# Optimization experiments

Measured on AMD Instinct MI355X. Metric: run time of the kernel, lower is better.

The kernel has to match this reference:

```python
import jax, jax.numpy as jnp
import numpy as np

N, D, M = 4096, 2048, 1000
NL = 2048
MAX_ITER = 5


def setup_inputs() -> dict:
    key = jax.random.key(0)
    k1, k2, k3 = jax.random.split(key, 3)
    fc7 = jax.random.normal(k1, (N, D), dtype=jnp.float32)
    # prior probs: softmax over random logits (row-stochastic, like CNN softmax output)
    probs = jax.nn.softmax(jax.random.normal(k2, (N, M), dtype=jnp.float32), axis=-1)
    labs = jax.random.randint(k3, (NL,), 0, M)
    L = jnp.arange(NL)
    U = jnp.arange(NL, N)
    return {"fc7": fc7, "probs": probs, "labs": labs, "L": L, "U": U}


def _get_W_correlation(fc7):
    # Pearson correlation between rows, negatives clipped to zero (set_negative='hard')
    x = fc7 - fc7.mean(axis=1, keepdims=True)
    norms = jnp.linalg.norm(x, axis=1)  # [n]
    W = (x @ x.T) / jnp.outer(norms, norms)  # [n, n]
    return jax.nn.relu(W)


def _init_probs_prior(probs, labs, L, U):
    n, m = probs.shape
    ps = jnp.zeros((n, m), dtype=probs.dtype)
    ps = ps.at[U].set(probs[U])       # unlabeled: CNN prior
    ps = ps.at[L, labs].set(1.0)      # labeled: one-hot
    return ps


def _replicator(W, ps, max_iter):
    def step(p, _):
        q = p * (W @ p)                              # [n, m]
        q = q / jnp.sum(q, axis=1, keepdims=True)
        return q, None
    ps, _ = jax.lax.scan(step, ps, None, length=max_iter)
    return ps


def reference(fc7, probs, labs, L, U):
    W = _get_W_correlation(fc7)
    ps = _init_probs_prior(probs, labs, L, U)
    ps = _replicator(W, ps, MAX_ITER)
    return ps, W
```

## Files before the change

kernel.cpp:

```cpp
#include <hip/hip_runtime.h>
#include <stdint.h>

#define NS 4096
#define DD 2048
#define MC 1000
#define MP 1024
#define NLAB 2048
#define NU 2048

typedef __attribute__((ext_vector_type(8))) short bf16x8;
typedef __attribute__((ext_vector_type(4))) float f32x4;

__device__ inline unsigned short f2bf(float f) {
  union { float f; uint32_t u; } v; v.f = f;
  uint32_t u = v.u;
  u = u + 0x7fffu + ((u >> 16) & 1u);
  return (unsigned short)(u >> 16);
}
__device__ inline float bf2f(unsigned short h) {
  union { uint32_t u; float f; } v; v.u = ((uint32_t)h) << 16;
  return v.f;
}

__device__ inline void gload_lds16(const void* g, void* l) {
  __builtin_amdgcn_global_load_lds(
      (const __attribute__((address_space(1))) void*)g,
      (__attribute__((address_space(3))) void*)l, 16, 0, 0);
}

__device__ inline float block_sum(float v, float* sm, int tid) {
  #pragma unroll
  for (int o = 32; o > 0; o >>= 1) v += __shfl_down(v, o, 64);
  __syncthreads();
  if ((tid & 63) == 0) sm[tid >> 6] = v;
  __syncthreads();
  return sm[0] + sm[1] + sm[2] + sm[3];
}

__global__ void center_norm_k(const float* __restrict__ fc7,
                              unsigned short* __restrict__ Xc,
                              float* __restrict__ invn) {
  __shared__ float sm[4];
  const int row = blockIdx.x;
  const int tid = threadIdx.x;
  const float4* src = (const float4*)(fc7 + (size_t)row * DD);
  float4 a = src[tid * 2];
  float4 b = src[tid * 2 + 1];
  float s = a.x + a.y + a.z + a.w + b.x + b.y + b.z + b.w;
  s = block_sum(s, sm, tid);
  const float mean = s * (1.f / (float)DD);
  float v0 = a.x - mean, v1 = a.y - mean, v2 = a.z - mean, v3 = a.w - mean;
  float v4 = b.x - mean, v5 = b.y - mean, v6 = b.z - mean, v7 = b.w - mean;
  float ss = v0*v0 + v1*v1 + v2*v2 + v3*v3 + v4*v4 + v5*v5 + v6*v6 + v7*v7;
  ss = block_sum(ss, sm, tid);
  if (tid == 0) invn[row] = rsqrtf(ss);
  ushort4 o0 = make_ushort4(f2bf(v0), f2bf(v1), f2bf(v2), f2bf(v3));
  ushort4 o1 = make_ushort4(f2bf(v4), f2bf(v5), f2bf(v6), f2bf(v7));
  ushort4* dst = (ushort4*)(Xc + (size_t)row * DD);
  dst[tid * 2] = o0;
  dst[tid * 2 + 1] = o1;
}

__global__ void gemm_w_sym(const unsigned short* __restrict__ A,
                           const float* __restrict__ invn,
                           float* __restrict__ outF,
                           unsigned short* __restrict__ outBF) {
  __shared__ __align__(16) unsigned short As[64 * 64];
  __shared__ __align__(16) unsigned short Bs[128 * 64];
  const int tid = threadIdx.x;
  const int wv = tid >> 6;
  const int ln = tid & 63;
  const int wr = wv >> 1, wc = wv & 1;

  int b = (blockIdx.x & 7) * 132 + (blockIdx.x >> 3);
  int r = 0;
  while (b >= 32 - (r >> 1)) { b -= 32 - (r >> 1); ++r; }
  const int c = (r >> 1) + b;
  const int rowBase = r * 64;
  const int colBase = c * 128;
  const bool mirror = (c > (r >> 1));
  const int fr = ln & 15, kg = ln >> 4;

  f32x4 acc[2][4];
  f32x4 zz = {0.f, 0.f, 0.f, 0.f};
  #pragma unroll
  for (int i = 0; i < 2; ++i)
    #pragma unroll
    for (int j = 0; j < 4; ++j) acc[i][j] = zz;

  const int lrow = ln >> 3;
  const int lcol = ((ln & 7) ^ lrow) * 8;
  const unsigned short* Ap = A + (size_t)(rowBase + lrow) * DD + lcol;
  const unsigned short* Bp = A + (size_t)(colBase + lrow) * DD + lcol;

  for (int k0 = 0; k0 < DD; k0 += 64) {
    if (k0) __syncthreads();
    #pragma unroll
    for (int u = 0; u < 2; ++u) {
      const int rr = wv * 16 + u * 8;
      gload_lds16(Ap + (size_t)rr * DD + k0, &As[rr * 64]);
    }
    #pragma unroll
    for (int u = 0; u < 4; ++u) {
      const int rr = wv * 32 + u * 8;
      gload_lds16(Bp + (size_t)rr * DD + k0, &Bs[rr * 64]);
    }
    __syncthreads();
    #pragma unroll
    for (int kk = 0; kk < 2; ++kk) {
      bf16x8 af[2], bfr[4];
      #pragma unroll
      for (int i = 0; i < 2; ++i) {
        const int rr = wr * 32 + i * 16 + fr;
        af[i] = *(const bf16x8*)&As[rr * 64 + ((kk * 4 + kg) ^ (rr & 7)) * 8];
      }
      #pragma unroll
      for (int j = 0; j < 4; ++j) {
        const int rr = wc * 64 + j * 16 + fr;
        bfr[j] = *(const bf16x8*)&Bs[rr * 64 + ((kk * 4 + kg) ^ (rr & 7)) * 8];
      }
      #pragma unroll
      for (int i = 0; i < 2; ++i)
        #pragma unroll
        for (int j = 0; j < 4; ++j)
          acc[i][j] = __builtin_amdgcn_mfma_f32_16x16x32_bf16(af[i], bfr[j], acc[i][j], 0, 0, 0);
    }
  }

  const int cr = (ln >> 4) * 4;
  const int cc = ln & 15;
  #pragma unroll
  for (int i = 0; i < 2; ++i) {
    const int rb = rowBase + wr * 32 + i * 16 + cr;
    #pragma unroll
    for (int j = 0; j < 4; ++j) {
      const int cb = colBase + wc * 64 + j * 16 + cc;
      const float ic = invn[cb];
      float v[4];
      #pragma unroll
      for (int u = 0; u < 4; ++u) {
        float x = acc[i][j][u] * invn[rb + u] * ic;
        v[u] = x > 0.f ? x : 0.f;
        const size_t o = (size_t)(rb + u) * NS + cb;
        outF[o] = v[u];
        outBF[o] = f2bf(v[u]);
      }
      if (mirror) {
        const size_t o = (size_t)cb * NS + rb;
        *(float4*)&outF[o] = make_float4(v[0], v[1], v[2], v[3]);
        *(ushort4*)&outBF[o] = make_ushort4(f2bf(v[0]), f2bf(v[1]), f2bf(v[2]), f2bf(v[3]));
      }
    }
  }
}

__global__ void gemm_rep(const unsigned short* __restrict__ pT,
                         const unsigned short* __restrict__ Wbf,
                         float* __restrict__ q0, float* __restrict__ q1,
                         float* __restrict__ q2, float* __restrict__ q3,
                         int kBase) {
  __shared__ __align__(16) unsigned short As[64 * 64];
  __shared__ __align__(16) unsigned short Bs[128 * 64];
  const int tid = threadIdx.x;
  const int wv = tid >> 6;
  const int ln = tid & 63;
  const int wr = wv >> 1, wc = wv & 1;
  const int rowBase = blockIdx.y * 64;
  const int colBase = blockIdx.x * 128;
  const int kOff = kBase + blockIdx.z * 512;
  float* __restrict__ outF = (blockIdx.z == 0) ? q0 : (blockIdx.z == 1) ? q1
                           : (blockIdx.z == 2) ? q2 : q3;
  const int fr = ln & 15, kg = ln >> 4;

  f32x4 acc[2][4];
  f32x4 zz = {0.f, 0.f, 0.f, 0.f};
  #pragma unroll
  for (int i = 0; i < 2; ++i)
    #pragma unroll
    for (int j = 0; j < 4; ++j) acc[i][j] = zz;

  const int lrow = ln >> 3;
  const int lcol = ((ln & 7) ^ lrow) * 8;
  const unsigned short* Ap = pT + (size_t)(rowBase + lrow) * NS + kOff + lcol;
  const unsigned short* Bp = Wbf + (size_t)(NLAB + colBase + lrow) * NS + kOff + lcol;

  for (int k0 = 0; k0 < 512; k0 += 64) {
    if (k0) __syncthreads();
    #pragma unroll
    for (int u = 0; u < 2; ++u) {
      const int rr = wv * 16 + u * 8;
      gload_lds16(Ap + (size_t)rr * NS + k0, &As[rr * 64]);
    }
    #pragma unroll
    for (int u = 0; u < 4; ++u) {
      const int rr = wv * 32 + u * 8;
      gload_lds16(Bp + (size_t)rr * NS + k0, &Bs[rr * 64]);
    }
    __syncthreads();
    #pragma unroll
    for (int kk = 0; kk < 2; ++kk) {
      bf16x8 af[2], bfr[4];
      #pragma unroll
      for (int i = 0; i < 2; ++i) {
        const int rr = wr * 32 + i * 16 + fr;
        af[i] = *(const bf16x8*)&As[rr * 64 + ((kk * 4 + kg) ^ (rr & 7)) * 8];
      }
      #pragma unroll
      for (int j = 0; j < 4; ++j) {
        const int rr = wc * 64 + j * 16 + fr;
        bfr[j] = *(const bf16x8*)&Bs[rr * 64 + ((kk * 4 + kg) ^ (rr & 7)) * 8];
      }
      #pragma unroll
      for (int i = 0; i < 2; ++i)
        #pragma unroll
        for (int j = 0; j < 4; ++j)
          acc[i][j] = __builtin_amdgcn_mfma_f32_16x16x32_bf16(af[i], bfr[j], acc[i][j], 0, 0, 0);
    }
  }

  const int cr = (ln >> 4) * 4;
  const int cc = ln & 15;
  #pragma unroll
  for (int i = 0; i < 2; ++i) {
    const int rb = rowBase + wr * 32 + i * 16 + cr;
    #pragma unroll
    for (int j = 0; j < 4; ++j) {
      const int cb = colBase + wc * 64 + j * 16 + cc;
      #pragma unroll
      for (int u = 0; u < 4; ++u)
        outF[(size_t)(rb + u) * NU + cb] = acc[i][j][u];
    }
  }
}

__global__ void merge_k(const float* __restrict__ q0, const float* __restrict__ q1,
                        const float* __restrict__ q2, const float* __restrict__ q3,
                        float* __restrict__ WL) {
  const int idx = (blockIdx.x * 256 + threadIdx.x) * 4;
  float4 a = *(const float4*)(q0 + idx);
  float4 b = *(const float4*)(q1 + idx);
  float4 c = *(const float4*)(q2 + idx);
  float4 d = *(const float4*)(q3 + idx);
  *(float4*)(WL + idx) = make_float4(a.x + b.x + c.x + d.x, a.y + b.y + c.y + d.y,
                                     a.z + b.z + c.z + d.z, a.w + b.w + c.w + d.w);
}

__global__ void init_pT_k(const float* __restrict__ probs, const int* __restrict__ labs,
                          unsigned short* __restrict__ pT) {
  __shared__ float t[32][33];
  const int tx = threadIdx.x, ty = threadIdx.y;
  const int i0 = blockIdx.x * 32, m0 = blockIdx.y * 32;
  const int i = i0 + ty;
  const int m = m0 + tx;
  float v = 0.f;
  if (i < NLAB) v = (m == labs[i]) ? 1.f : 0.f;
  else if (m < MC) v = probs[(size_t)i * MC + m];
  t[ty][tx] = v;
  __syncthreads();
  pT[(size_t)(m0 + ty) * NS + i0 + tx] = f2bf(t[tx][ty]);
}

__global__ void onehot_k(const int* __restrict__ labs, float* __restrict__ ps) {
  const int i = blockIdx.x;
  const int m4 = threadIdx.x * 4;
  if (m4 >= MC) return;
  const int lab = labs[i];
  float4 v;
  v.x = (lab == m4)     ? 1.f : 0.f;
  v.y = (lab == m4 + 1) ? 1.f : 0.f;
  v.z = (lab == m4 + 2) ? 1.f : 0.f;
  v.w = (lab == m4 + 3) ? 1.f : 0.f;
  *(float4*)&ps[(size_t)i * MC + m4] = v;
}

__global__ void colsum_part_k(const float* __restrict__ q0, const float* __restrict__ q1,
                              const float* __restrict__ q2, const float* __restrict__ q3,
                              const float* __restrict__ WL,
                              const unsigned short* __restrict__ pT,
                              float* __restrict__ pq,
                              float* __restrict__ part) {
  const int i = blockIdx.x * 256 + threadIdx.x;
  const int c = blockIdx.y;
  float s = 0.f;
  #pragma unroll 4
  for (int mm = 0; mm < 64; ++mm) {
    const int m = c * 64 + mm;
    const size_t o = (size_t)m * NU + i;
    const float q = q0[o] + q1[o] + q2[o] + q3[o] + WL[o];
    const float f = bf2f(pT[(size_t)m * NS + NLAB + i]) * q;
    s += f;
    pq[o] = f;
  }
  part[c * NU + i] = s;
}

__global__ void colsum_fin_k(const float* __restrict__ part, float* __restrict__ rsum) {
  const int i = blockIdx.x * 256 + threadIdx.x;
  float s = 0.f;
  #pragma unroll
  for (int c = 0; c < 16; ++c) s += part[c * NU + i];
  rsum[i] = 1.0f / s;
}

__global__ void scale_k(const float* __restrict__ pq,
                        const float* __restrict__ rsum,
                        unsigned short* __restrict__ pT) {
  const int g = blockIdx.x * 256 + threadIdx.x;
  const int idx = g * 4;
  const int i = idx & (NU - 1);
  const int m = idx >> 11;
  float4 p = *(const float4*)(pq + idx);
  float4 r = *(const float4*)(rsum + i);
  ushort4 o = make_ushort4(f2bf(p.x * r.x), f2bf(p.y * r.y),
                           f2bf(p.z * r.z), f2bf(p.w * r.w));
  *(ushort4*)(pT + (size_t)m * NS + NLAB + i) = o;
}

__global__ void final_k(const float* __restrict__ pq,
                        const float* __restrict__ rsum,
                        float* __restrict__ ps) {
  __shared__ float t[32][33];
  const int tx = threadIdx.x, ty = threadIdx.y;
  const int i0 = blockIdx.x * 32, m0 = blockIdx.y * 32;
  t[ty][tx] = pq[(size_t)(m0 + ty) * NU + i0 + tx];
  __syncthreads();
  const int i = i0 + ty, m = m0 + tx;
  if (m < MC)
    ps[(size_t)(NLAB + i) * MC + m] = t[tx][ty] * rsum[i];
}

extern "C" void kernel_launch(void* const* d_in, const int* in_sizes, int n_in,
                              void* d_out, int out_size, void* d_ws, size_t ws_size,
                              hipStream_t stream) {
  const float* fc7   = (const float*)d_in[0];
  const float* probs = (const float*)d_in[1];
  const int*   labs  = (const int*)d_in[2];

  char* ws = (char*)d_ws;
  unsigned short* Xc   = (unsigned short*)(ws);
  unsigned short* Wbf  = (unsigned short*)(ws + (16ull << 20));
  unsigned short* pT   = (unsigned short*)(ws + (48ull << 20));
  float*          q0   = (float*)(ws + (56ull << 20));
  float*          q1   = (float*)(ws + (64ull << 20));
  float*          q2   = (float*)(ws + (72ull << 20));
  float*          q3   = (float*)(ws + (80ull << 20));
  float*          WL   = (float*)(ws + (88ull << 20));
  float*          pq   = (float*)(ws + (96ull << 20));
  float*          invn = (float*)(ws + (104ull << 20));
  float*          rsum = (float*)(ws + (104ull << 20) + (16ull << 10));
  float*          part = (float*)(ws + (104ull << 20) + (32ull << 10));

  float* out_ps = (float*)d_out;
  float* out_W  = out_ps + (size_t)NS * MC;

  center_norm_k<<<NS, 256, 0, stream>>>(fc7, Xc, invn);

  gemm_w_sym<<<1056, 256, 0, stream>>>(Xc, invn, out_W, Wbf);

  init_pT_k<<<dim3(NS / 32, MP / 32), dim3(32, 32), 0, stream>>>(probs, labs, pT);
  onehot_k<<<NLAB, 256, 0, stream>>>(labs, out_ps);

  gemm_rep<<<dim3(NU / 128, MP / 64, 4), 256, 0, stream>>>(pT, Wbf, q0, q1, q2, q3, 0);
  merge_k<<<(MP * NU / 4) / 256, 256, 0, stream>>>(q0, q1, q2, q3, WL);

  for (int it = 0; it < 5; ++it) {
    gemm_rep<<<dim3(NU / 128, MP / 64, 4), 256, 0, stream>>>(pT, Wbf, q0, q1, q2, q3, NLAB);
    colsum_part_k<<<dim3(NU / 256, 16), 256, 0, stream>>>(q0, q1, q2, q3, WL, pT, pq, part);
    colsum_fin_k<<<NU / 256, 256, 0, stream>>>(part, rsum);
    if (it < 4)
      scale_k<<<(MP * NU / 4) / 256, 256, 0, stream>>>(pq, rsum, pT);
    else
      final_k<<<dim3(NU / 32, MP / 32), dim3(32, 32), 0, stream>>>(pq, rsum, out_ps);
  }
}
```

Measured before the change: 282.3 us.

## Replace labeled-part GEMM with label-bucketed gather-sum of W rows

The labeled rows of p are one-hot, so the labeled contribution W_UL @ p_L is computed by bucketing labels (count, scan, stable rank-scatter) and summing the matching bf16 W rows per class, instead of running a full split-K GEMM followed by a merge. This removes a 2048-deep GEMM pass and the merge kernel and replaces them with several small kernels plus a gather. Separately, colsum_part_k now uses 64 column chunks of 16 instead of 16 chunks of 64, giving more parallelism at the cost of a longer final reduction. The rank step is quadratic in the label count, and its summation order differs from the GEMM accumulation.

```diff
diff --git a/kernel.cpp b/kernel.cpp
--- a/kernel.cpp
+++ b/kernel.cpp
@@ -233,16 +233,58 @@
   }
 }
 
-__global__ void merge_k(const float* __restrict__ q0, const float* __restrict__ q1,
-                        const float* __restrict__ q2, const float* __restrict__ q3,
-                        float* __restrict__ WL) {
-  const int idx = (blockIdx.x * 256 + threadIdx.x) * 4;
-  float4 a = *(const float4*)(q0 + idx);
-  float4 b = *(const float4*)(q1 + idx);
-  float4 c = *(const float4*)(q2 + idx);
-  float4 d = *(const float4*)(q3 + idx);
-  *(float4*)(WL + idx) = make_float4(a.x + b.x + c.x + d.x, a.y + b.y + c.y + d.y,
-                                     a.z + b.z + c.z + d.z, a.w + b.w + c.w + d.w);
+__global__ void count_k(const int* __restrict__ labs, int* __restrict__ counts) {
+  const int j = blockIdx.x * 256 + threadIdx.x;
+  atomicAdd(&counts[labs[j]], 1);
+}
+
+__global__ void scan_k(const int* __restrict__ counts, int* __restrict__ offsets) {
+  __shared__ int s[1024];
+  const int t = threadIdx.x;
+  s[t] = counts[t];
+  __syncthreads();
+  #pragma unroll
+  for (int o = 1; o < 1024; o <<= 1) {
+    int v = (t >= o) ? s[t - o] : 0;
+    __syncthreads();
+    s[t] += v;
+    __syncthreads();
+  }
+  offsets[t] = s[t] - counts[t];
+}
+
+__global__ void rank_scatter_k(const int* __restrict__ labs,
+                               const int* __restrict__ offsets,
+                               int* __restrict__ idx) {
+  __shared__ int ll[NLAB];
+  const int t = threadIdx.x;
+  for (int u = t; u < NLAB; u += 256) ll[u] = labs[u];
+  __syncthreads();
+  const int j = blockIdx.x * 256 + t;
+  const int lab = ll[j];
+  int rank = 0;
+  for (int jp = 0; jp < j; ++jp) rank += (ll[jp] == lab);
+  idx[offsets[lab] + rank] = j;
+}
+
+__global__ void wl_gather_k(const int* __restrict__ counts, const int* __restrict__ offsets,
+                            const int* __restrict__ idx,
+                            const unsigned short* __restrict__ Wbf,
+                            float* __restrict__ WL) {
+  const int m = blockIdx.x;
+  const int t = threadIdx.x;
+  const int cnt = counts[m];
+  const int off = offsets[m];
+  float acc[8] = {0.f, 0.f, 0.f, 0.f, 0.f, 0.f, 0.f, 0.f};
+  for (int b = 0; b < cnt; ++b) {
+    const int j = idx[off + b];
+    bf16x8 w = *(const bf16x8*)&Wbf[(size_t)j * NS + NLAB + t * 8];
+    #pragma unroll
+    for (int k = 0; k < 8; ++k) acc[k] += bf2f((unsigned short)w[k]);
+  }
+  float* dst = WL + (size_t)m * NU + t * 8;
+  *(float4*)dst = make_float4(acc[0], acc[1], acc[2], acc[3]);
+  *(float4*)(dst + 4) = make_float4(acc[4], acc[5], acc[6], acc[7]);
 }
 
 __global__ void init_pT_k(const float* __restrict__ probs, const int* __restrict__ labs,
@@ -283,8 +325,8 @@
   const int c = blockIdx.y;
   float s = 0.f;
   #pragma unroll 4
-  for (int mm = 0; mm < 64; ++mm) {
-    const int m = c * 64 + mm;
+  for (int mm = 0; mm < 16; ++mm) {
+    const int m = c * 16 + mm;
     const size_t o = (size_t)m * NU + i;
     const float q = q0[o] + q1[o] + q2[o] + q3[o] + WL[o];
     const float f = bf2f(pT[(size_t)m * NS + NLAB + i]) * q;
@@ -298,7 +340,7 @@
   const int i = blockIdx.x * 256 + threadIdx.x;
   float s = 0.f;
   #pragma unroll
-  for (int c = 0; c < 16; ++c) s += part[c * NU + i];
+  for (int c = 0; c < 64; ++c) s += part[c * NU + i];
   rsum[i] = 1.0f / s;
 }
 
@@ -348,7 +390,10 @@
   float*          pq   = (float*)(ws + (96ull << 20));
   float*          invn = (float*)(ws + (104ull << 20));
   float*          rsum = (float*)(ws + (104ull << 20) + (16ull << 10));
-  float*          part = (float*)(ws + (104ull << 20) + (32ull << 10));
+  float*          part = (float*)(ws + (105ull << 20));
+  int*            cnts = (int*)(ws + (106ull << 20));
+  int*            offs = (int*)(ws + (106ull << 20) + (4ull << 10));
+  int*            idx  = (int*)(ws + (106ull << 20) + (8ull << 10));
 
   float* out_ps = (float*)d_out;
   float* out_W  = out_ps + (size_t)NS * MC;
@@ -360,12 +405,15 @@
   init_pT_k<<<dim3(NS / 32, MP / 32), dim3(32, 32), 0, stream>>>(probs, labs, pT);
   onehot_k<<<NLAB, 256, 0, stream>>>(labs, out_ps);
 
-  gemm_rep<<<dim3(NU / 128, MP / 64, 4), 256, 0, stream>>>(pT, Wbf, q0, q1, q2, q3, 0);
-  merge_k<<<(MP * NU / 4) / 256, 256, 0, stream>>>(q0, q1, q2, q3, WL);
+  hipMemsetAsync(cnts, 0, 1024 * sizeof(int), stream);
+  count_k<<<NLAB / 256, 256, 0, stream>>>(labs, cnts);
+  scan_k<<<1, 1024, 0, stream>>>(cnts, offs);
+  rank_scatter_k<<<NLAB / 256, 256, 0, stream>>>(labs, offs, idx);
+  wl_gather_k<<<MP, 256, 0, stream>>>(cnts, offs, idx, Wbf, WL);
 
   for (int it = 0; it < 5; ++it) {
     gemm_rep<<<dim3(NU / 128, MP / 64, 4), 256, 0, stream>>>(pT, Wbf, q0, q1, q2, q3, NLAB);
-    colsum_part_k<<<dim3(NU / 256, 16), 256, 0, stream>>>(q0, q1, q2, q3, WL, pT, pq, part);
+    colsum_part_k<<<dim3(NU / 256, 64), 256, 0, stream>>>(q0, q1, q2, q3, WL, pT, pq, part);
     colsum_fin_k<<<NU / 256, 256, 0, stream>>>(part, rsum);
     if (it < 4)
       scale_k<<<(MP * NU / 4) / 256, 256, 0, stream>>>(pq, rsum, pT);
```

Measured after the change: 380.6 us. 34.8% more time.

## Replace labeled-row GEMM with one-hot gather of W columns; widen colsum split

Applied to the files above, without the earlier changes.

The constant contribution of the labeled (one-hot) rows to W@p is now built by a gather kernel. For each class it sums the W rows of the labels that belong to that class, replacing a full split-K GEMM pass over the labeled half plus a merge kernel. It exploits the one-hot structure of the labeled priors, so the result stays exact and does not depend on the inputs. The column-sum partial kernel is also split into 64 chunks instead of 16 to raise parallelism, at the cost of a larger partial buffer and more work in the final reduction. The gather kernel scans all 2048 labels in every one of its 1024 blocks, a serial loop that may itself be slow.

```diff
diff --git a/kernel.cpp b/kernel.cpp
--- a/kernel.cpp
+++ b/kernel.cpp
@@ -233,16 +233,27 @@
   }
 }
 
-__global__ void merge_k(const float* __restrict__ q0, const float* __restrict__ q1,
-                        const float* __restrict__ q2, const float* __restrict__ q3,
-                        float* __restrict__ WL) {
-  const int idx = (blockIdx.x * 256 + threadIdx.x) * 4;
-  float4 a = *(const float4*)(q0 + idx);
-  float4 b = *(const float4*)(q1 + idx);
-  float4 c = *(const float4*)(q2 + idx);
-  float4 d = *(const float4*)(q3 + idx);
-  *(float4*)(WL + idx) = make_float4(a.x + b.x + c.x + d.x, a.y + b.y + c.y + d.y,
-                                     a.z + b.z + c.z + d.z, a.w + b.w + c.w + d.w);
+__global__ void wl_gather_k(const int* __restrict__ labs,
+                            const unsigned short* __restrict__ Wbf,
+                            float* __restrict__ WL) {
+  __shared__ int ll[NLAB];
+  const int m = blockIdx.x;
+  const int t = threadIdx.x;
+  for (int u = t; u < NLAB / 4; u += 256)
+    ((int4*)ll)[u] = ((const int4*)labs)[u];
+  __syncthreads();
+  float acc[8] = {0.f, 0.f, 0.f, 0.f, 0.f, 0.f, 0.f, 0.f};
+  #pragma unroll 8
+  for (int j = 0; j < NLAB; ++j) {
+    if (ll[j] == m) {
+      bf16x8 w = *(const bf16x8*)&Wbf[(size_t)j * NS + NLAB + t * 8];
+      #pragma unroll
+      for (int k = 0; k < 8; ++k) acc[k] += bf2f((unsigned short)w[k]);
+    }
+  }
+  float* dst = WL + (size_t)m * NU + t * 8;
+  *(float4*)dst = make_float4(acc[0], acc[1], acc[2], acc[3]);
+  *(float4*)(dst + 4) = make_float4(acc[4], acc[5], acc[6], acc[7]);
 }
 
 __global__ void init_pT_k(const float* __restrict__ probs, const int* __restrict__ labs,
@@ -283,8 +294,8 @@
   const int c = blockIdx.y;
   float s = 0.f;
   #pragma unroll 4
-  for (int mm = 0; mm < 64; ++mm) {
-    const int m = c * 64 + mm;
+  for (int mm = 0; mm < 16; ++mm) {
+    const int m = c * 16 + mm;
     const size_t o = (size_t)m * NU + i;
     const float q = q0[o] + q1[o] + q2[o] + q3[o] + WL[o];
     const float f = bf2f(pT[(size_t)m * NS + NLAB + i]) * q;
@@ -298,7 +309,7 @@
   const int i = blockIdx.x * 256 + threadIdx.x;
   float s = 0.f;
   #pragma unroll
-  for (int c = 0; c < 16; ++c) s += part[c * NU + i];
+  for (int c = 0; c < 64; ++c) s += part[c * NU + i];
   rsum[i] = 1.0f / s;
 }
 
@@ -348,7 +359,7 @@
   float*          pq   = (float*)(ws + (96ull << 20));
   float*          invn = (float*)(ws + (104ull << 20));
   float*          rsum = (float*)(ws + (104ull << 20) + (16ull << 10));
-  float*          part = (float*)(ws + (104ull << 20) + (32ull << 10));
+  float*          part = (float*)(ws + (105ull << 20));
 
   float* out_ps = (float*)d_out;
   float* out_W  = out_ps + (size_t)NS * MC;
@@ -360,12 +371,11 @@
   init_pT_k<<<dim3(NS / 32, MP / 32), dim3(32, 32), 0, stream>>>(probs, labs, pT);
   onehot_k<<<NLAB, 256, 0, stream>>>(labs, out_ps);
 
-  gemm_rep<<<dim3(NU / 128, MP / 64, 4), 256, 0, stream>>>(pT, Wbf, q0, q1, q2, q3, 0);
-  merge_k<<<(MP * NU / 4) / 256, 256, 0, stream>>>(q0, q1, q2, q3, WL);
+  wl_gather_k<<<MP, 256, 0, stream>>>(labs, Wbf, WL);
 
   for (int it = 0; it < 5; ++it) {
     gemm_rep<<<dim3(NU / 128, MP / 64, 4), 256, 0, stream>>>(pT, Wbf, q0, q1, q2, q3, NLAB);
-    colsum_part_k<<<dim3(NU / 256, 16), 256, 0, stream>>>(q0, q1, q2, q3, WL, pT, pq, part);
+    colsum_part_k<<<dim3(NU / 256, 64), 256, 0, stream>>>(q0, q1, q2, q3, WL, pT, pq, part);
     colsum_fin_k<<<NU / 256, 256, 0, stream>>>(part, rsum);
     if (it < 4)
       scale_k<<<(MP * NU / 4) / 256, 256, 0, stream>>>(pq, rsum, pT);
```

Measured after the change: 408.8 us. 1.45x slower.
